# Kernel optimization log

Measured on AMD Instinct MI355X. Metric: run time of the kernel, lower is better.

The kernel has to match this reference:

```python
import jax, jax.numpy as jnp
import numpy as np

EPS = 1e-08


def setup_inputs() -> dict:
    key = jax.random.key(0)
    k1, k2, k3, k4 = jax.random.split(key, 4)
    src_len, bsz, d = 2048, 32, 1024
    inp = {
        "input": jax.random.normal(k1, (bsz, d), dtype=jnp.float32),
        "source_hids": jax.random.normal(k2, (src_len, bsz, d), dtype=jnp.float32),
        "encoder_padding_mask": jnp.zeros((src_len, bsz), dtype=bool),
        "W_in": jax.random.normal(k3, (d, d), dtype=jnp.float32) * (d ** -0.5),
        "W_out": jax.random.normal(k4, (d, 2 * d), dtype=jnp.float32) * ((2 * d) ** -0.5),
    }
    return inp


def reference(input, source_hids, encoder_padding_mask, W_in, W_out):
    # ProductEnergyLayer (scale=False): energy = sum_d source_hids * (input @ W_in^T)
    x = input @ W_in.T  # [bsz, ctx]
    energy = jnp.einsum("sbd,bd->sb", source_hids, x)  # [src_len, bsz]
    energy = jnp.where(encoder_padding_mask, -1e9, energy)

    # p_choose = sigmoid(monotonic energy)
    p = jax.nn.sigmoid(energy)  # [src_len, bsz]

    # exclusive cumprod of (1 - p) along src_len
    one_minus_p = 1.0 - p
    ones_row = jnp.ones_like(p[:1])
    cumprod_1mp = jnp.cumprod(jnp.concatenate([ones_row, one_minus_p[:-1]], axis=0), axis=0)

    denominator = jnp.clip(cumprod_1mp, EPS, 1.0)

    # previous_attention defaults to one-hot at position 0
    prev_attn = jnp.zeros_like(p).at[0].set(1.0)

    # alpha = p * cumprod(1-p) * cumsum(prev / cumprod(1-p))
    alpha = p * cumprod_1mp * jnp.cumsum(prev_attn / denominator, axis=0)

    # monotonic_type == 'hard' -> beta = alpha
    beta = alpha

    # weighted context and output projection
    weighted_context = jnp.einsum("sbd,sb->bd", source_hids, beta)  # [bsz, ctx]
    output = jnp.tanh(jnp.concatenate([weighted_context, input], axis=1) @ W_out.T)
    return output, beta, alpha
```

## Files before the change

kernel.cpp:

```cpp
#include <hip/hip_runtime.h>
#include <hip/hip_bf16.h>
#include <math.h>


#define SRC_LEN 2048
#define BSZ     32
#define DIM     1024
#define CH      64
#define TAIL4   ((SRC_LEN - CH) * BSZ / 4)

__global__ __launch_bounds__(256) void k_xproj(const float* __restrict__ input,
                                               const float* __restrict__ W,
                                               float* __restrict__ x) {
    int wid  = blockIdx.x * 4 + (threadIdx.x >> 6);
    int lane = threadIdx.x & 63;
    int b    = wid >> 6;
    int i0   = (wid & 63) * 16;
    const float4* inp = (const float4*)(input + (size_t)b * DIM);
    float4 in[4];
    #pragma unroll
    for (int k = 0; k < 4; ++k) in[k] = inp[lane + 64 * k];
    #pragma unroll 4
    for (int i = 0; i < 16; ++i) {
        const float4* wr = (const float4*)(W + (size_t)(i0 + i) * DIM);
        float acc = 0.f;
        #pragma unroll
        for (int k = 0; k < 4; ++k) {
            float4 wv = wr[lane + 64 * k];
            acc += wv.x * in[k].x + wv.y * in[k].y + wv.z * in[k].z + wv.w * in[k].w;
        }
        #pragma unroll
        for (int off = 32; off; off >>= 1) acc += __shfl_down(acc, off);
        if (lane == 0) x[(size_t)b * DIM + i0 + i] = acc;
    }
}

__global__ __launch_bounds__(256) void k_energy_fill(const float* __restrict__ src,
                                                     const float* __restrict__ x,
                                                     float* __restrict__ energy,
                                                     float* __restrict__ beta_out,
                                                     float* __restrict__ alpha_out) {
    int bid = blockIdx.x;
    if (bid < 512) {
        int wid  = bid * 4 + (threadIdx.x >> 6);
        int lane = threadIdx.x & 63;
        int s = wid >> 5, b = wid & (BSZ - 1);
        const float4* row = (const float4*)(src + ((size_t)s * BSZ + b) * DIM);
        const float4* xr  = (const float4*)(x + (size_t)b * DIM);
        float acc = 0.f;
        #pragma unroll
        for (int k = 0; k < 4; ++k) {
            float4 v = row[lane + 64 * k];
            float4 c = xr[lane + 64 * k];
            acc += v.x * c.x + v.y * c.y + v.z * c.z + v.w * c.w;
        }
        #pragma unroll
        for (int off = 32; off; off >>= 1) acc += __shfl_down(acc, off);
        if (lane == 0) energy[(size_t)s * BSZ + b] = acc;
    } else {
        int i = (bid - 512) * 256 + threadIdx.x;
        if (i < TAIL4) {
            float4 z = {0.f, 0.f, 0.f, 0.f};
            ((float4*)(beta_out  + (size_t)CH * BSZ))[i] = z;
            ((float4*)(alpha_out + (size_t)CH * BSZ))[i] = z;
        }
    }
}

__global__ __launch_bounds__(1024) void k_scan_wc(const float* __restrict__ src,
                                                  const float* __restrict__ x,
                                                  const unsigned char* __restrict__ mask,
                                                  const float* __restrict__ energy,
                                                  float* __restrict__ beta_out,
                                                  float* __restrict__ alpha_out,
                                                  float* __restrict__ wc) {
    int b = blockIdx.x;
    int t = threadIdx.x;
    int w = t >> 6, lane = t & 63;
    __shared__ float pb[CH];
    __shared__ int   snz;
    __shared__ float cstate;
    __shared__ float red[16];
    __shared__ float crun, bcur;
    __shared__ __align__(16) float xs[DIM];

    if (w == 0) {
        float ev = energy[(size_t)lane * BSZ + b];
        if (mask[(size_t)lane * BSZ + b]) ev = -1e9f;
        float p  = 1.0f / (1.0f + expf(-ev));
        float om = 1.0f - p;
        float prod = om;
        #pragma unroll
        for (int off = 1; off < 64; off <<= 1) {
            float o = __shfl_up(prod, off);
            if (lane >= off) prod *= o;
        }
        float excl = __shfl_up(prod, 1);
        if (lane == 0) excl = 1.0f;
        float a = p * excl;
        beta_out[(size_t)lane * BSZ + b]  = a;
        alpha_out[(size_t)lane * BSZ + b] = a;
        pb[lane] = a;
        unsigned long long nz = __ballot(a != 0.0f);
        if (lane == 0) snz = (nz == 0ULL) ? 0 : (64 - __builtin_clzll(nz));
        if (lane == 63) cstate = prod;
    }
    __syncthreads();

    float acc = 0.f;
    int smax = snz;
    for (int s = 0; s < smax; ++s) {
        float wgt = pb[s];
        if (wgt != 0.0f) acc += wgt * src[((size_t)s * BSZ + b) * DIM + t];
    }

    if (cstate != 0.0f) {
        for (int i = t; i < DIM; i += 1024) xs[i] = x[(size_t)b * DIM + i];
        if (t == 0) crun = cstate;
        __syncthreads();
        for (int s = CH; s < SRC_LEN; ++s) {
            float v = src[((size_t)s * BSZ + b) * DIM + t];
            float part = v * xs[t];
            #pragma unroll
            for (int off = 32; off; off >>= 1) part += __shfl_down(part, off);
            if (lane == 0) red[w] = part;
            __syncthreads();
            if (t == 0) {
                float ev = 0.f;
                #pragma unroll
                for (int i = 0; i < 16; ++i) ev += red[i];
                if (mask[(size_t)s * BSZ + b]) ev = -1e9f;
                float p = 1.0f / (1.0f + expf(-ev));
                float a = p * crun;
                beta_out[(size_t)s * BSZ + b]  = a;
                alpha_out[(size_t)s * BSZ + b] = a;
                bcur = a;
                crun = crun * (1.0f - p);
            }
            __syncthreads();
            acc += bcur * v;
            if (crun == 0.0f) break;
        }
    }

    wc[(size_t)b * DIM + t] = acc;
}

__global__ __launch_bounds__(256) void k_out(const float* __restrict__ wc,
                                             const float* __restrict__ input,
                                             const float* __restrict__ W,
                                             float* __restrict__ out) {
    int wid  = blockIdx.x * 4 + (threadIdx.x >> 6);
    int lane = threadIdx.x & 63;
    int b    = wid >> 6;
    int o0   = (wid & 63) * 16;
    const float4* wcp = (const float4*)(wc    + (size_t)b * DIM);
    const float4* inp = (const float4*)(input + (size_t)b * DIM);
    float4 c[4], u[4];
    #pragma unroll
    for (int k = 0; k < 4; ++k) {
        c[k] = wcp[lane + 64 * k];
        u[k] = inp[lane + 64 * k];
    }
    #pragma unroll 4
    for (int i = 0; i < 16; ++i) {
        const float4* wr = (const float4*)(W + (size_t)(o0 + i) * 2 * DIM);
        float acc = 0.f;
        #pragma unroll
        for (int k = 0; k < 4; ++k) {
            float4 wv = wr[lane + 64 * k];
            acc += wv.x * c[k].x + wv.y * c[k].y + wv.z * c[k].z + wv.w * c[k].w;
        }
        #pragma unroll
        for (int k = 0; k < 4; ++k) {
            float4 wv = wr[256 + lane + 64 * k];
            acc += wv.x * u[k].x + wv.y * u[k].y + wv.z * u[k].z + wv.w * u[k].w;
        }
        #pragma unroll
        for (int off = 32; off; off >>= 1) acc += __shfl_down(acc, off);
        if (lane == 0) out[(size_t)b * DIM + o0 + i] = tanhf(acc);
    }
}

extern "C" void kernel_launch(void* const* d_in, const int* in_sizes, int n_in,
                              void* d_out, int out_size, void* d_ws, size_t ws_size,
                              hipStream_t stream) {
    const float* input = (const float*)d_in[0];
    const float* src   = (const float*)d_in[1];
    const unsigned char* mask = (const unsigned char*)d_in[2];
    const float* W_in  = (const float*)d_in[3];
    const float* W_out = (const float*)d_in[4];

    float* out_proj  = (float*)d_out;
    float* beta_out  = out_proj + BSZ * DIM;
    float* alpha_out = beta_out + SRC_LEN * BSZ;

    float* ws = (float*)d_ws;
    float* x      = ws;
    float* wc     = x + BSZ * DIM;
    float* energy = wc + BSZ * DIM;

    k_xproj<<<512, 256, 0, stream>>>(input, W_in, x);
    k_energy_fill<<<512 + 64, 256, 0, stream>>>(src, x, energy, beta_out, alpha_out);
    k_scan_wc<<<BSZ, 1024, 0, stream>>>(src, x, mask, energy, beta_out, alpha_out, wc);
    k_out<<<512, 256, 0, stream>>>(wc, input, W_out, out_proj);
}
```

Measured before the change: 30.57 us.

## Fuse input projection with first-chunk energy partials into one front kernel

Merges the x-projection and the energy kernel into one launch. Each wave, right after computing its 16 projected features, multiplies them against the matching 16-element slice of source_hids for the first 64 source positions and writes partial energies. The scan kernel then sums 64 partials per position instead of reading a finished energy. This removes one kernel launch and the dependency round trip through x, at the cost of extra partial-sum storage and a 64-term reduction in the scan's first wave.

```diff
diff --git a/kernel.cpp b/kernel.cpp
--- a/kernel.cpp
+++ b/kernel.cpp
@@ -8,69 +8,67 @@
 #define DIM     1024
 #define CH      64
 #define TAIL4   ((SRC_LEN - CH) * BSZ / 4)
-
-__global__ __launch_bounds__(256) void k_xproj(const float* __restrict__ input,
-                                               const float* __restrict__ W,
-                                               float* __restrict__ x) {
-    int wid  = blockIdx.x * 4 + (threadIdx.x >> 6);
-    int lane = threadIdx.x & 63;
-    int b    = wid >> 6;
-    int i0   = (wid & 63) * 16;
-    const float4* inp = (const float4*)(input + (size_t)b * DIM);
-    float4 in[4];
-    #pragma unroll
-    for (int k = 0; k < 4; ++k) in[k] = inp[lane + 64 * k];
-    #pragma unroll 4
-    for (int i = 0; i < 16; ++i) {
-        const float4* wr = (const float4*)(W + (size_t)(i0 + i) * DIM);
-        float acc = 0.f;
+#define XPB     512
+#define FILLB   (TAIL4 / 256)
+#define NB1     (XPB + FILLB)
+
+__global__ __launch_bounds__(256) void k_front(const float* __restrict__ input,
+                                               const float* __restrict__ W_in,
+                                               const float* __restrict__ src,
+                                               float* __restrict__ x,
+                                               float* __restrict__ epart,
+                                               float* __restrict__ beta_out,
+                                               float* __restrict__ alpha_out) {
+    int bid = blockIdx.x;
+    int t = threadIdx.x;
+    int lane = t & 63;
+    if (bid < XPB) {
+        int wid = bid * 4 + (t >> 6);
+        int b   = wid >> 6;
+        int ic  = wid & 63;
+        int i0  = ic * 16;
+        const float4* inp = (const float4*)(input + (size_t)b * DIM);
+        float4 in[4];
+        #pragma unroll
+        for (int k = 0; k < 4; ++k) in[k] = inp[lane + 64 * k];
+        float accs[16];
+        #pragma unroll 4
+        for (int i = 0; i < 16; ++i) {
+            const float4* wr = (const float4*)(W_in + (size_t)(i0 + i) * DIM);
+            float acc = 0.f;
+            #pragma unroll
+            for (int k = 0; k < 4; ++k) {
+                float4 wv = wr[lane + 64 * k];
+                acc += wv.x * in[k].x + wv.y * in[k].y + wv.z * in[k].z + wv.w * in[k].w;
+            }
+            #pragma unroll
+            for (int off = 32; off; off >>= 1) acc += __shfl_down(acc, off);
+            accs[i] = acc;
+            if (lane == 0) x[(size_t)b * DIM + i0 + i] = acc;
+        }
+        const float4* sp = (const float4*)(src + ((size_t)lane * BSZ + b) * DIM + i0);
+        float pe = 0.f;
         #pragma unroll
         for (int k = 0; k < 4; ++k) {
-            float4 wv = wr[lane + 64 * k];
-            acc += wv.x * in[k].x + wv.y * in[k].y + wv.z * in[k].z + wv.w * in[k].w;
-        }
-        #pragma unroll
-        for (int off = 32; off; off >>= 1) acc += __shfl_down(acc, off);
-        if (lane == 0) x[(size_t)b * DIM + i0 + i] = acc;
-    }
-}
-
-__global__ __launch_bounds__(256) void k_energy_fill(const float* __restrict__ src,
-                                                     const float* __restrict__ x,
-                                                     float* __restrict__ energy,
-                                                     float* __restrict__ beta_out,
-                                                     float* __restrict__ alpha_out) {
-    int bid = blockIdx.x;
-    if (bid < 512) {
-        int wid  = bid * 4 + (threadIdx.x >> 6);
-        int lane = threadIdx.x & 63;
-        int s = wid >> 5, b = wid & (BSZ - 1);
-        const float4* row = (const float4*)(src + ((size_t)s * BSZ + b) * DIM);
-        const float4* xr  = (const float4*)(x + (size_t)b * DIM);
-        float acc = 0.f;
-        #pragma unroll
-        for (int k = 0; k < 4; ++k) {
-            float4 v = row[lane + 64 * k];
-            float4 c = xr[lane + 64 * k];
-            acc += v.x * c.x + v.y * c.y + v.z * c.z + v.w * c.w;
-        }
-        #pragma unroll
-        for (int off = 32; off; off >>= 1) acc += __shfl_down(acc, off);
-        if (lane == 0) energy[(size_t)s * BSZ + b] = acc;
+            float4 v = sp[k];
+            pe += v.x * __shfl(accs[4 * k + 0], 0)
+                + v.y * __shfl(accs[4 * k + 1], 0)
+                + v.z * __shfl(accs[4 * k + 2], 0)
+                + v.w * __shfl(accs[4 * k + 3], 0);
+        }
+        epart[(size_t)ic * (BSZ * CH) + b * CH + lane] = pe;
     } else {
-        int i = (bid - 512) * 256 + threadIdx.x;
-        if (i < TAIL4) {
-            float4 z = {0.f, 0.f, 0.f, 0.f};
-            ((float4*)(beta_out  + (size_t)CH * BSZ))[i] = z;
-            ((float4*)(alpha_out + (size_t)CH * BSZ))[i] = z;
-        }
+        int i = (bid - XPB) * 256 + t;
+        float4 z = {0.f, 0.f, 0.f, 0.f};
+        ((float4*)(beta_out  + (size_t)CH * BSZ))[i] = z;
+        ((float4*)(alpha_out + (size_t)CH * BSZ))[i] = z;
     }
 }
 
 __global__ __launch_bounds__(1024) void k_scan_wc(const float* __restrict__ src,
                                                   const float* __restrict__ x,
                                                   const unsigned char* __restrict__ mask,
-                                                  const float* __restrict__ energy,
+                                                  const float* __restrict__ epart,
                                                   float* __restrict__ beta_out,
                                                   float* __restrict__ alpha_out,
                                                   float* __restrict__ wc) {
@@ -85,7 +83,10 @@
     __shared__ __align__(16) float xs[DIM];
 
     if (w == 0) {
-        float ev = energy[(size_t)lane * BSZ + b];
+        float ev = 0.f;
+        #pragma unroll
+        for (int c = 0; c < 64; ++c)
+            ev += epart[(size_t)c * (BSZ * CH) + b * CH + lane];
         if (mask[(size_t)lane * BSZ + b]) ev = -1e9f;
         float p  = 1.0f / (1.0f + expf(-ev));
         float om = 1.0f - p;
@@ -196,12 +197,11 @@
     float* alpha_out = beta_out + SRC_LEN * BSZ;
 
     float* ws = (float*)d_ws;
-    float* x      = ws;
-    float* wc     = x + BSZ * DIM;
-    float* energy = wc + BSZ * DIM;
-
-    k_xproj<<<512, 256, 0, stream>>>(input, W_in, x);
-    k_energy_fill<<<512 + 64, 256, 0, stream>>>(src, x, energy, beta_out, alpha_out);
-    k_scan_wc<<<BSZ, 1024, 0, stream>>>(src, x, mask, energy, beta_out, alpha_out, wc);
+    float* x     = ws;
+    float* wc    = x + BSZ * DIM;
+    float* epart = wc + BSZ * DIM;
+
+    k_front<<<NB1, 256, 0, stream>>>(input, W_in, src, x, epart, beta_out, alpha_out);
+    k_scan_wc<<<BSZ, 1024, 0, stream>>>(src, x, mask, epart, beta_out, alpha_out, wc);
     k_out<<<512, 256, 0, stream>>>(wc, input, W_out, out_proj);
 }
```

Result: slower. 42.33 us (+38.5%).
